# Kernel tuning notes

Measured on AMD Instinct MI355X. Metric: run time of the kernel, lower is better.

The kernel has to match this reference:

```python
import jax, jax.numpy as jnp
import numpy as np

INPUT_DIM = 784
LATENT_DIM = 32
HIDDEN = 256
NUM_PROTO = 25  # 5x5 SOM grid
BATCH = 65536


def setup_inputs() -> dict:
    key = jax.random.key(0)
    ks = jax.random.split(key, 10)
    s = lambda fan_in: 1.0 / np.sqrt(fan_in)
    return {
        "x": jax.random.uniform(ks[0], (BATCH, INPUT_DIM), dtype=jnp.float32),
        # encoder: Linear(784,256) -> ReLU -> Linear(256,32)
        "We1": jax.random.normal(ks[1], (INPUT_DIM, HIDDEN), dtype=jnp.float32) * s(INPUT_DIM),
        "be1": jnp.zeros((HIDDEN,), dtype=jnp.float32),
        "We2": jax.random.normal(ks[2], (HIDDEN, LATENT_DIM), dtype=jnp.float32) * s(HIDDEN),
        "be2": jnp.zeros((LATENT_DIM,), dtype=jnp.float32),
        # decoder: Linear(32,256) -> ReLU -> Linear(256,784) -> Sigmoid
        "Wd1": jax.random.normal(ks[3], (LATENT_DIM, HIDDEN), dtype=jnp.float32) * s(LATENT_DIM),
        "bd1": jnp.zeros((HIDDEN,), dtype=jnp.float32),
        "Wd2": jax.random.normal(ks[4], (HIDDEN, INPUT_DIM), dtype=jnp.float32) * s(HIDDEN),
        "bd2": jnp.zeros((INPUT_DIM,), dtype=jnp.float32),
        # SOM prototypes (torch.randn init)
        "prototypes": jax.random.normal(ks[5], (NUM_PROTO, LATENT_DIM), dtype=jnp.float32),
    }


def reference(x, We1, be1, We2, be2, Wd1, bd1, Wd2, bd2, prototypes):
    # encoder
    h = jax.nn.relu(x @ We1 + be1)          # [B, 256]
    z = h @ We2 + be2                        # [B, 32]
    # SOM layer: cdist -> argmin -> gather winning prototype
    # squared euclidean distance suffices for argmin
    sq_dists = (jnp.sum(z * z, axis=1, keepdims=True)
                - 2.0 * (z @ prototypes.T)
                + jnp.sum(prototypes * prototypes, axis=1))  # [B, 25]
    min_idx = jnp.argmin(sq_dists, axis=1)   # [B]
    som_z = prototypes[min_idx]              # [B, 32]
    # decoder
    hd = jax.nn.relu(som_z @ Wd1 + bd1)      # [B, 256]
    x_recon = jax.nn.sigmoid(hd @ Wd2 + bd2)  # [B, 784]
    return (x_recon, z, som_z)
```

## Files before the change

### kernel.cpp

```cpp
#include <hip/hip_runtime.h>
#include <hip/hip_bf16.h>
#include <math.h>

#define BATCH   65536
#define IN_DIM  784
#define HID     256
#define LAT     32
#define NPROTO  25

typedef short  short8  __attribute__((ext_vector_type(8)));
typedef float  floatx4 __attribute__((ext_vector_type(4)));

__device__ __forceinline__ unsigned short f2bf(float v) {
    __hip_bfloat16 b = __float2bfloat16(v);
    return *reinterpret_cast<unsigned short*>(&b);
}
__device__ __forceinline__ float bf2f(unsigned short u) {
    __hip_bfloat16 b = *reinterpret_cast<__hip_bfloat16*>(&u);
    return __bfloat162float(b);
}
__device__ __forceinline__ void split3(float v, unsigned short& o1,
                                       unsigned short& o2, unsigned short& o3) {
    o1 = f2bf(v); float r1 = v - bf2f(o1);
    o2 = f2bf(r1); float r2 = r1 - bf2f(o2);
    o3 = f2bf(r2);
}

__device__ __forceinline__ floatx4 mm_bf16(short8 a, short8 b, floatx4 c) {
    return __builtin_amdgcn_mfma_f32_16x16x32_bf16(a, b, c, 0, 0, 0);
}

__device__ __forceinline__ void async_copy16(const void* g, void* l) {
    __builtin_amdgcn_global_load_lds(
        (const __attribute__((address_space(1))) unsigned int*)g,
        (__attribute__((address_space(3))) unsigned int*)l, 16, 0, 0);
}

#define BT_BYTES   409600
#define WS_NEEDED  1307200

__global__ __launch_bounds__(256)
void prep_B(const float* __restrict__ We1,
            unsigned short* __restrict__ B1,
            unsigned short* __restrict__ B2,
            unsigned short* __restrict__ B3)
{
    int e = (blockIdx.x * 256 + threadIdx.x) * 4;
    int k = e & 31;
    int n = (e >> 5) & 255;
    int s = e >> 13;
    int cs = (k >> 3) ^ ((n >> 1) & 3);
    int dst = (s * 256 + n) * 32 + cs * 8 + (k & 7);
    ushort4 u1, u2, u3;
    unsigned short a, b, c;
#pragma unroll
    for (int j = 0; j < 4; ++j) {
        int kk = s * 32 + k + j;
        float v = (kk < IN_DIM) ? We1[(size_t)kk * HID + n] : 0.f;
        split3(v, a, b, c);
        ((unsigned short*)&u1)[j] = a;
        ((unsigned short*)&u2)[j] = b;
        ((unsigned short*)&u3)[j] = c;
    }
    *(ushort4*)(B1 + dst) = u1;
    *(ushort4*)(B2 + dst) = u2;
    *(ushort4*)(B3 + dst) = u3;
}

__global__ __launch_bounds__(256)
void dpsom_dectab(const float* __restrict__ protos,
                  const float* __restrict__ Wd1,
                  const float* __restrict__ bd1,
                  const float* __restrict__ Wd2,
                  const float* __restrict__ bd2,
                  float* __restrict__ table)
{
    __shared__ float pr[LAT];
    __shared__ float hd[HID];
    const int p = blockIdx.x;
    const int tid = threadIdx.x;
    if (tid < LAT) pr[tid] = protos[p * LAT + tid];
    __syncthreads();
    float s = bd1[tid];
#pragma unroll
    for (int k = 0; k < LAT; ++k)
        s = fmaf(pr[k], Wd1[k * HID + tid], s);
    hd[tid] = fmaxf(s, 0.f);
    __syncthreads();
    for (int i = tid; i < IN_DIM; i += 256) {
        float o = bd2[i];
        for (int j = 0; j < HID; ++j)
            o = fmaf(hd[j], Wd2[(size_t)j * IN_DIM + i], o);
        table[p * IN_DIM + i] = 1.f / (1.f + expf(-o));
    }
}

__global__ __launch_bounds__(256, 2)
void dpsom_encoder_mfma(const float* __restrict__ x,
                        const unsigned short* __restrict__ B1g,
                        const unsigned short* __restrict__ B2g,
                        const unsigned short* __restrict__ B3g,
                        const float* __restrict__ be1,
                        const float* __restrict__ We2,
                        const float* __restrict__ be2,
                        const float* __restrict__ protos,
                        const float* __restrict__ table,
                        float* __restrict__ z_out,
                        float* __restrict__ somz_out,
                        float* __restrict__ xrec)
{
    __shared__ __align__(16) char smem[61440];
    const int tid  = threadIdx.x;
    const int wave = tid >> 6;
    const int lane = tid & 63;
    const int l15  = lane & 15;
    const int q    = lane >> 4;
    const int sw   = (l15 >> 1) & 3;
    const int row0 = blockIdx.x * 64;

    floatx4 acc[4][4];
#pragma unroll
    for (int i = 0; i < 4; ++i)
#pragma unroll
        for (int j = 0; j < 4; ++j) acc[i][j] = (floatx4)0.f;

    for (int s = 0; s < 25; ++s) {
        __syncthreads();
        {
            size_t gbase = (size_t)s * 16384 + (size_t)wave * 4096 + (size_t)lane * 16;
            char* lb = smem + 12288 + wave * 4096 + lane * 16;
#pragma unroll
            for (int i = 0; i < 4; ++i) {
                async_copy16((const char*)B1g + gbase + i * 1024, lb + 0     + i * 1024);
                async_copy16((const char*)B2g + gbase + i * 1024, lb + 16384 + i * 1024);
                async_copy16((const char*)B3g + gbase + i * 1024, lb + 32768 + i * 1024);
            }
        }
#pragma unroll
        for (int i = 0; i < 2; ++i) {
            int ff  = tid + i * 256;
            int row = ff >> 3;
            int k4  = ff & 7;
            float4 v = make_float4(0.f, 0.f, 0.f, 0.f);
            if (s < 24 || k4 < 4)
                v = *(const float4*)(x + (size_t)(row0 + row) * IN_DIM + s * 32 + k4 * 4);
            ushort4 u1, u2, u3;
            unsigned short a, b, c;
            split3(v.x, a, b, c); u1.x = a; u2.x = b; u3.x = c;
            split3(v.y, a, b, c); u1.y = a; u2.y = b; u3.y = c;
            split3(v.z, a, b, c); u1.z = a; u2.z = b; u3.z = c;
            split3(v.w, a, b, c); u1.w = a; u2.w = b; u3.w = c;
            int csw = ((k4 >> 1) ^ ((row >> 1) & 3));
            int dst = row * 64 + csw * 16 + (k4 & 1) * 8;
            *(ushort4*)(smem + dst)        = u1;
            *(ushort4*)(smem + 4096 + dst) = u2;
            *(ushort4*)(smem + 8192 + dst) = u3;
        }
        __syncthreads();

        short8 afr[3][4];
#pragma unroll
        for (int mf = 0; mf < 4; ++mf) {
            int abyte = (16 * mf + l15) * 64 + ((q ^ sw) * 16);
            afr[0][mf] = *(short8*)(smem + abyte);
            afr[1][mf] = *(short8*)(smem + 4096 + abyte);
            afr[2][mf] = *(short8*)(smem + 8192 + abyte);
        }
#pragma unroll
        for (int nf = 0; nf < 4; ++nf) {
            int n = wave * 64 + 16 * nf + l15;
            int bbyte = n * 64 + ((q ^ sw) * 16);
            short8 b1 = *(short8*)(smem + 12288 + bbyte);
            short8 b2 = *(short8*)(smem + 28672 + bbyte);
            short8 b3 = *(short8*)(smem + 45056 + bbyte);
#pragma unroll
            for (int mf = 0; mf < 4; ++mf) {
                floatx4 t = acc[mf][nf];
                t = mm_bf16(afr[0][mf], b1, t);
                t = mm_bf16(afr[0][mf], b2, t);
                t = mm_bf16(afr[1][mf], b1, t);
                t = mm_bf16(afr[1][mf], b2, t);
                t = mm_bf16(afr[0][mf], b3, t);
                t = mm_bf16(afr[2][mf], b1, t);
                acc[mf][nf] = t;
            }
        }
    }

    {
        float bias[4];
#pragma unroll
        for (int nf = 0; nf < 4; ++nf) bias[nf] = be1[wave * 64 + 16 * nf + l15];
#pragma unroll
        for (int mf = 0; mf < 4; ++mf)
#pragma unroll
            for (int nf = 0; nf < 4; ++nf)
#pragma unroll
                for (int r = 0; r < 4; ++r)
                    acc[mf][nf][r] = fmaxf(acc[mf][nf][r] + bias[nf], 0.f);
    }

    float* h_lds = (float*)smem;
    float* z_lds = (float*)(smem + 33280);
    int*  minidx = (int*)(smem + 41728);

    const int jz = tid & 31;
    const int rg = tid >> 5;
    const float bz = be2[jz];

    for (int half = 0; half < 2; ++half) {
        __syncthreads();
#pragma unroll
        for (int mm = 0; mm < 2; ++mm) {
            int mf = 2 * half + mm;
#pragma unroll
            for (int nf = 0; nf < 4; ++nf)
#pragma unroll
                for (int r = 0; r < 4; ++r) {
                    int lr = 16 * mm + 4 * q + r;
                    h_lds[lr * 260 + wave * 64 + 16 * nf + l15] = acc[mf][nf][r];
                }
        }
        __syncthreads();
        float s0 = bz, s1 = bz, s2 = bz, s3 = bz;
        const float* h0p = h_lds + (rg * 4 + 0) * 260;
        const float* h1p = h_lds + (rg * 4 + 1) * 260;
        const float* h2p = h_lds + (rg * 4 + 2) * 260;
        const float* h3p = h_lds + (rg * 4 + 3) * 260;
#pragma unroll 4
        for (int c = 0; c < HID; c += 4) {
            float w0 = We2[(c + 0) * LAT + jz];
            float w1 = We2[(c + 1) * LAT + jz];
            float w2 = We2[(c + 2) * LAT + jz];
            float w3 = We2[(c + 3) * LAT + jz];
            float4 h0 = *(const float4*)(h0p + c);
            float4 h1 = *(const float4*)(h1p + c);
            float4 h2 = *(const float4*)(h2p + c);
            float4 h3 = *(const float4*)(h3p + c);
            s0 = fmaf(h0.x, w0, fmaf(h0.y, w1, fmaf(h0.z, w2, fmaf(h0.w, w3, s0))));
            s1 = fmaf(h1.x, w0, fmaf(h1.y, w1, fmaf(h1.z, w2, fmaf(h1.w, w3, s1))));
            s2 = fmaf(h2.x, w0, fmaf(h2.y, w1, fmaf(h2.z, w2, fmaf(h2.w, w3, s2))));
            s3 = fmaf(h3.x, w0, fmaf(h3.y, w1, fmaf(h3.z, w2, fmaf(h3.w, w3, s3))));
        }
        int rbase = half * 32 + rg * 4;
        z_lds[(rbase + 0) * 33 + jz] = s0;
        z_lds[(rbase + 1) * 33 + jz] = s1;
        z_lds[(rbase + 2) * 33 + jz] = s2;
        z_lds[(rbase + 3) * 33 + jz] = s3;
        z_out[(size_t)(row0 + rbase + 0) * LAT + jz] = s0;
        z_out[(size_t)(row0 + rbase + 1) * LAT + jz] = s1;
        z_out[(size_t)(row0 + rbase + 2) * LAT + jz] = s2;
        z_out[(size_t)(row0 + rbase + 3) * LAT + jz] = s3;
    }
    __syncthreads();

    if (tid < 64) {
        float zr[LAT];
        float zn = 0.f;
#pragma unroll
        for (int j = 0; j < LAT; ++j) {
            zr[j] = z_lds[tid * 33 + j];
            zn = fmaf(zr[j], zr[j], zn);
        }
        float best = 3.4e38f;
        int bp = 0;
        for (int p = 0; p < NPROTO; ++p) {
            float dot = 0.f, pn = 0.f;
#pragma unroll
            for (int j = 0; j < LAT; ++j) {
                float pv = protos[p * LAT + j];
                dot = fmaf(zr[j], pv, dot);
                pn  = fmaf(pv, pv, pn);
            }
            float d = zn - 2.f * dot + pn;
            if (d < best) { best = d; bp = p; }
        }
        minidx[tid] = bp;
    }
    __syncthreads();

#pragma unroll
    for (int m = 0; m < 8; ++m) {
        int r = rg * 8 + m;
        somz_out[(size_t)(row0 + r) * LAT + jz] = protos[minidx[r] * LAT + jz];
    }

    for (int i2 = tid; i2 < 64 * 196; i2 += 256) {
        int row = i2 / 196;
        int c   = i2 - row * 196;
        int idx = minidx[row];
        ((float4*)xrec)[(size_t)(row0 + row) * 196 + c] =
            ((const float4*)table)[idx * 196 + c];
    }
}

#define BMf 64
#define BKf 16
#define HSTRIDE 260
#define ZSTRIDE 33
#define SMEM_FLOATS 10432

__global__ __launch_bounds__(256)
void dpsom_encoder_fp32(const float* __restrict__ x,
                        const float* __restrict__ We1,
                        const float* __restrict__ be1,
                        const float* __restrict__ We2,
                        const float* __restrict__ be2,
                        const float* __restrict__ protos,
                        float* __restrict__ z_out,
                        float* __restrict__ somz_out,
                        int* __restrict__ minidx_out)
{
    __shared__ float smem[SMEM_FLOATS];
    __shared__ int minidx_lds[BMf];
    float* As = smem;
    float* Bs = smem + BKf * BMf;
    float* h_lds = smem;
    float* z_lds = smem + 32 * HSTRIDE;

    const int tid = threadIdx.x;
    const int tx = tid & 31;
    const int ty = tid >> 5;
    const int row0 = blockIdx.x * BMf;

    float acc[8][8];
#pragma unroll
    for (int i = 0; i < 8; ++i)
#pragma unroll
        for (int j = 0; j < 8; ++j) acc[i][j] = 0.f;

    const int ar  = tid >> 2;
    const int akq = tid & 3;

    for (int k0 = 0; k0 < IN_DIM; k0 += BKf) {
        __syncthreads();
        float4 av = *(const float4*)(x + (size_t)(row0 + ar) * IN_DIM + k0 + akq * 4);
        As[(akq * 4 + 0) * BMf + ar] = av.x;
        As[(akq * 4 + 1) * BMf + ar] = av.y;
        As[(akq * 4 + 2) * BMf + ar] = av.z;
        As[(akq * 4 + 3) * BMf + ar] = av.w;
#pragma unroll
        for (int i = 0; i < 4; ++i) {
            int f  = tid + i * 256;
            int bk = f >> 6;
            int bn = (f & 63) << 2;
            *(float4*)(Bs + bk * HID + bn) =
                *(const float4*)(We1 + (size_t)(k0 + bk) * HID + bn);
        }
        __syncthreads();
#pragma unroll
        for (int kk = 0; kk < BKf; ++kk) {
            float4 a0 = *(const float4*)(As + kk * BMf + ty * 8);
            float4 a1 = *(const float4*)(As + kk * BMf + ty * 8 + 4);
            float4 b0 = *(const float4*)(Bs + kk * HID + tx * 8);
            float4 b1 = *(const float4*)(Bs + kk * HID + tx * 8 + 4);
            float a[8] = {a0.x, a0.y, a0.z, a0.w, a1.x, a1.y, a1.z, a1.w};
            float b[8] = {b0.x, b0.y, b0.z, b0.w, b1.x, b1.y, b1.z, b1.w};
#pragma unroll
            for (int i = 0; i < 8; ++i)
#pragma unroll
                for (int j = 0; j < 8; ++j)
                    acc[i][j] = fmaf(a[i], b[j], acc[i][j]);
        }
    }
    {
        float bias[8];
#pragma unroll
        for (int j = 0; j < 8; ++j) bias[j] = be1[tx * 8 + j];
#pragma unroll
        for (int i = 0; i < 8; ++i)
#pragma unroll
            for (int j = 0; j < 8; ++j)
                acc[i][j] = fmaxf(acc[i][j] + bias[j], 0.f);
    }
    const int jz = tid & 31;
    const int rg = tid >> 5;
    const float bz = be2[jz];
    for (int half = 0; half < 2; ++half) {
        __syncthreads();
        if ((ty >> 2) == half) {
            int rb = (ty & 3) * 8;
#pragma unroll
            for (int i = 0; i < 8; ++i) {
                *(float4*)(h_lds + (rb + i) * HSTRIDE + tx * 8) =
                    make_float4(acc[i][0], acc[i][1], acc[i][2], acc[i][3]);
                *(float4*)(h_lds + (rb + i) * HSTRIDE + tx * 8 + 4) =
                    make_float4(acc[i][4], acc[i][5], acc[i][6], acc[i][7]);
            }
        }
        __syncthreads();
        float s0 = bz, s1 = bz, s2 = bz, s3 = bz;
        const float* h0p = h_lds + (rg * 4 + 0) * HSTRIDE;
        const float* h1p = h_lds + (rg * 4 + 1) * HSTRIDE;
        const float* h2p = h_lds + (rg * 4 + 2) * HSTRIDE;
        const float* h3p = h_lds + (rg * 4 + 3) * HSTRIDE;
#pragma unroll 4
        for (int c = 0; c < HID; c += 4) {
            float w0 = We2[(c + 0) * LAT + jz];
            float w1 = We2[(c + 1) * LAT + jz];
            float w2 = We2[(c + 2) * LAT + jz];
            float w3 = We2[(c + 3) * LAT + jz];
            float4 h0 = *(const float4*)(h0p + c);
            float4 h1 = *(const float4*)(h1p + c);
            float4 h2 = *(const float4*)(h2p + c);
            float4 h3 = *(const float4*)(h3p + c);
            s0 = fmaf(h0.x, w0, fmaf(h0.y, w1, fmaf(h0.z, w2, fmaf(h0.w, w3, s0))));
            s1 = fmaf(h1.x, w0, fmaf(h1.y, w1, fmaf(h1.z, w2, fmaf(h1.w, w3, s1))));
            s2 = fmaf(h2.x, w0, fmaf(h2.y, w1, fmaf(h2.z, w2, fmaf(h2.w, w3, s2))));
            s3 = fmaf(h3.x, w0, fmaf(h3.y, w1, fmaf(h3.z, w2, fmaf(h3.w, w3, s3))));
        }
        int rbase = half * 32 + rg * 4;
        z_lds[(rbase + 0) * ZSTRIDE + jz] = s0;
        z_lds[(rbase + 1) * ZSTRIDE + jz] = s1;
        z_lds[(rbase + 2) * ZSTRIDE + jz] = s2;
        z_lds[(rbase + 3) * ZSTRIDE + jz] = s3;
        z_out[(size_t)(row0 + rbase + 0) * LAT + jz] = s0;
        z_out[(size_t)(row0 + rbase + 1) * LAT + jz] = s1;
        z_out[(size_t)(row0 + rbase + 2) * LAT + jz] = s2;
        z_out[(size_t)(row0 + rbase + 3) * LAT + jz] = s3;
    }
    __syncthreads();
    if (tid < BMf) {
        float zr[LAT];
        float zn = 0.f;
#pragma unroll
        for (int j = 0; j < LAT; ++j) {
            zr[j] = z_lds[tid * ZSTRIDE + j];
            zn = fmaf(zr[j], zr[j], zn);
        }
        float best = 3.4e38f;
        int bp = 0;
        for (int p = 0; p < NPROTO; ++p) {
            float dot = 0.f, pn = 0.f;
#pragma unroll
            for (int j = 0; j < LAT; ++j) {
                float pv = protos[p * LAT + j];
                dot = fmaf(zr[j], pv, dot);
                pn  = fmaf(pv, pv, pn);
            }
            float d = zn - 2.f * dot + pn;
            if (d < best) { best = d; bp = p; }
        }
        minidx_out[row0 + tid] = bp;
        minidx_lds[tid] = bp;
    }
    __syncthreads();
#pragma unroll
    for (int m = 0; m < 8; ++m) {
        int r = rg * 8 + m;
        somz_out[(size_t)(row0 + r) * LAT + jz] = protos[minidx_lds[r] * LAT + jz];
    }
}

__global__ __launch_bounds__(256)
void dpsom_gather(const float4* __restrict__ table,
                  const int* __restrict__ minidx,
                  float4* __restrict__ xrec)
{
    const int f = blockIdx.x * 256 + threadIdx.x;
    const int row = f / 196;
    const int c4  = f - row * 196;
    const int idx = minidx[row];
    xrec[f] = table[idx * 196 + c4];
}

extern "C" void kernel_launch(void* const* d_in, const int* in_sizes, int n_in,
                              void* d_out, int out_size, void* d_ws, size_t ws_size,
                              hipStream_t stream)
{
    const float* x    = (const float*)d_in[0];
    const float* We1  = (const float*)d_in[1];
    const float* be1  = (const float*)d_in[2];
    const float* We2  = (const float*)d_in[3];
    const float* be2  = (const float*)d_in[4];
    const float* Wd1  = (const float*)d_in[5];
    const float* bd1  = (const float*)d_in[6];
    const float* Wd2  = (const float*)d_in[7];
    const float* bd2  = (const float*)d_in[8];
    const float* prot = (const float*)d_in[9];

    float* out   = (float*)d_out;
    float* xrec  = out;
    float* z_out = out + (size_t)BATCH * IN_DIM;
    float* somz  = z_out + (size_t)BATCH * LAT;

    if (ws_size >= WS_NEEDED) {
        unsigned short* B1 = (unsigned short*)d_ws;
        unsigned short* B2 = (unsigned short*)((char*)d_ws + BT_BYTES);
        unsigned short* B3 = (unsigned short*)((char*)d_ws + 2 * BT_BYTES);
        float* table = (float*)((char*)d_ws + 3 * BT_BYTES);

        hipLaunchKernelGGL(prep_B, dim3(200), dim3(256), 0, stream, We1, B1, B2, B3);
        hipLaunchKernelGGL(dpsom_dectab, dim3(NPROTO), dim3(256), 0, stream,
                           prot, Wd1, bd1, Wd2, bd2, table);
        hipLaunchKernelGGL(dpsom_encoder_mfma, dim3(BATCH / 64), dim3(256), 0, stream,
                           x, B1, B2, B3, be1, We2, be2, prot, table,
                           z_out, somz, xrec);
    } else {
        int*   minidx = (int*)d_ws;
        float* table  = (float*)((char*)d_ws + (size_t)BATCH * 4);
        hipLaunchKernelGGL(dpsom_encoder_fp32, dim3(BATCH / BMf), dim3(256), 0, stream,
                           x, We1, be1, We2, be2, prot, z_out, somz, minidx);
        hipLaunchKernelGGL(dpsom_dectab, dim3(NPROTO), dim3(256), 0, stream,
                           prot, Wd1, bd1, Wd2, bd2, table);
        hipLaunchKernelGGL(dpsom_gather, dim3((BATCH * (IN_DIM / 4)) / 256), dim3(256), 0, stream,
                           (const float4*)table, minidx, (float4*)xrec);
    }
}
```

Measured before the change: 516.0 us.

## Stream B fragments from global into registers and double-buffer A tiles in LDS

```diff
diff --git a/kernel.cpp b/kernel.cpp
--- a/kernel.cpp
+++ b/kernel.cpp
@@ -30,41 +30,37 @@
     return __builtin_amdgcn_mfma_f32_16x16x32_bf16(a, b, c, 0, 0, 0);
 }
 
-__device__ __forceinline__ void async_copy16(const void* g, void* l) {
-    __builtin_amdgcn_global_load_lds(
-        (const __attribute__((address_space(1))) unsigned int*)g,
-        (__attribute__((address_space(3))) unsigned int*)l, 16, 0, 0);
-}
-
-#define BT_BYTES   409600
+#define BT_SHORTS  204800
 #define WS_NEEDED  1307200
 
 __global__ __launch_bounds__(256)
-void prep_B(const float* __restrict__ We1,
-            unsigned short* __restrict__ B1,
-            unsigned short* __restrict__ B2,
-            unsigned short* __restrict__ B3)
+void prep_BF(const float* __restrict__ We1,
+             unsigned short* __restrict__ B1,
+             unsigned short* __restrict__ B2,
+             unsigned short* __restrict__ B3)
 {
-    int e = (blockIdx.x * 256 + threadIdx.x) * 4;
-    int k = e & 31;
-    int n = (e >> 5) & 255;
-    int s = e >> 13;
-    int cs = (k >> 3) ^ ((n >> 1) & 3);
-    int dst = (s * 256 + n) * 32 + cs * 8 + (k & 7);
-    ushort4 u1, u2, u3;
-    unsigned short a, b, c;
-#pragma unroll
-    for (int j = 0; j < 4; ++j) {
-        int kk = s * 32 + k + j;
-        float v = (kk < IN_DIM) ? We1[(size_t)kk * HID + n] : 0.f;
+    int t   = blockIdx.x * 256 + threadIdx.x;
+    int l15 = t & 15;
+    int q   = (t >> 4) & 3;
+    int sn  = t >> 6;
+    int s   = sn >> 4;
+    int n   = (sn & 15) * 16 + l15;
+    int k0  = s * 32 + q * 8;
+    short8 v1, v2, v3;
+#pragma unroll
+    for (int j = 0; j < 8; ++j) {
+        int k = k0 + j;
+        float v = (k < IN_DIM) ? We1[(size_t)k * HID + n] : 0.f;
+        unsigned short a, b, c;
         split3(v, a, b, c);
-        ((unsigned short*)&u1)[j] = a;
-        ((unsigned short*)&u2)[j] = b;
-        ((unsigned short*)&u3)[j] = c;
-    }
-    *(ushort4*)(B1 + dst) = u1;
-    *(ushort4*)(B2 + dst) = u2;
-    *(ushort4*)(B3 + dst) = u3;
+        v1[j] = (short)a;
+        v2[j] = (short)b;
+        v3[j] = (short)c;
+    }
+    size_t o = (size_t)t * 8;
+    *(short8*)(B1 + o) = v1;
+    *(short8*)(B2 + o) = v2;
+    *(short8*)(B3 + o) = v3;
 }
 
 __global__ __launch_bounds__(256)
@@ -95,96 +91,119 @@
     }
 }
 
-__global__ __launch_bounds__(256, 2)
-void dpsom_encoder_mfma(const float* __restrict__ x,
-                        const unsigned short* __restrict__ B1g,
-                        const unsigned short* __restrict__ B2g,
-                        const unsigned short* __restrict__ B3g,
-                        const float* __restrict__ be1,
-                        const float* __restrict__ We2,
-                        const float* __restrict__ be2,
-                        const float* __restrict__ protos,
-                        const float* __restrict__ table,
-                        float* __restrict__ z_out,
-                        float* __restrict__ somz_out,
-                        float* __restrict__ xrec)
+#define AST  80
+#define ABUF 15360
+
+__device__ __forceinline__ void cvt_write3(float4 v0, float4 v1, char* wp) {
+    float vv[8] = {v0.x, v0.y, v0.z, v0.w, v1.x, v1.y, v1.z, v1.w};
+    short8 u1, u2, u3;
+#pragma unroll
+    for (int j = 0; j < 8; ++j) {
+        unsigned short a, b, c;
+        split3(vv[j], a, b, c);
+        u1[j] = (short)a;
+        u2[j] = (short)b;
+        u3[j] = (short)c;
+    }
+    *(short8*)(wp)          = u1;
+    *(short8*)(wp + 5120)   = u2;
+    *(short8*)(wp + 10240)  = u3;
+}
+
+__global__ __launch_bounds__(256, 3)
+void dpsom_encoder_bf3(const float* __restrict__ x,
+                       const unsigned short* __restrict__ B1g,
+                       const unsigned short* __restrict__ B2g,
+                       const unsigned short* __restrict__ B3g,
+                       const float* __restrict__ be1,
+                       const float* __restrict__ We2,
+                       const float* __restrict__ be2,
+                       const float* __restrict__ protos,
+                       const float* __restrict__ table,
+                       float* __restrict__ z_out,
+                       float* __restrict__ somz_out,
+                       float* __restrict__ xrec)
 {
-    __shared__ __align__(16) char smem[61440];
+    __shared__ __align__(16) char smem[45056];
     const int tid  = threadIdx.x;
     const int wave = tid >> 6;
     const int lane = tid & 63;
     const int l15  = lane & 15;
     const int q    = lane >> 4;
-    const int sw   = (l15 >> 1) & 3;
     const int row0 = blockIdx.x * 64;
 
+    const int arow = tid >> 2;
+    const int aq   = tid & 3;
+    const float* xrow = x + (size_t)(row0 + arow) * IN_DIM + aq * 8;
+    char* awp = smem + arow * AST + aq * 16;
+
     floatx4 acc[4][4];
 #pragma unroll
     for (int i = 0; i < 4; ++i)
 #pragma unroll
         for (int j = 0; j < 4; ++j) acc[i][j] = (floatx4)0.f;
 
+    {
+        float4 v0 = *(const float4*)(xrow);
+        float4 v1 = *(const float4*)(xrow + 4);
+        cvt_write3(v0, v1, awp);
+    }
+    __syncthreads();
+
     for (int s = 0; s < 25; ++s) {
-        __syncthreads();
+        const char* abase = smem + (s & 1) * ABUF;
+        const int fb = (s * 16 + wave * 4) << 9;
+
+        short8 b1, b2, b3;
         {
-            size_t gbase = (size_t)s * 16384 + (size_t)wave * 4096 + (size_t)lane * 16;
-            char* lb = smem + 12288 + wave * 4096 + lane * 16;
-#pragma unroll
-            for (int i = 0; i < 4; ++i) {
-                async_copy16((const char*)B1g + gbase + i * 1024, lb + 0     + i * 1024);
-                async_copy16((const char*)B2g + gbase + i * 1024, lb + 16384 + i * 1024);
-                async_copy16((const char*)B3g + gbase + i * 1024, lb + 32768 + i * 1024);
+            int off0 = fb + (lane << 3);
+            b1 = *(const short8*)(B1g + off0);
+            b2 = *(const short8*)(B2g + off0);
+            b3 = *(const short8*)(B3g + off0);
+        }
+
+        float4 v0 = make_float4(0.f, 0.f, 0.f, 0.f), v1 = v0;
+        if (s < 24) {
+            if ((s < 23) | (aq < 2)) {
+                v0 = *(const float4*)(xrow + (s + 1) * 32);
+                v1 = *(const float4*)(xrow + (s + 1) * 32 + 4);
             }
         }
-#pragma unroll
-        for (int i = 0; i < 2; ++i) {
-            int ff  = tid + i * 256;
-            int row = ff >> 3;
-            int k4  = ff & 7;
-            float4 v = make_float4(0.f, 0.f, 0.f, 0.f);
-            if (s < 24 || k4 < 4)
-                v = *(const float4*)(x + (size_t)(row0 + row) * IN_DIM + s * 32 + k4 * 4);
-            ushort4 u1, u2, u3;
-            unsigned short a, b, c;
-            split3(v.x, a, b, c); u1.x = a; u2.x = b; u3.x = c;
-            split3(v.y, a, b, c); u1.y = a; u2.y = b; u3.y = c;
-            split3(v.z, a, b, c); u1.z = a; u2.z = b; u3.z = c;
-            split3(v.w, a, b, c); u1.w = a; u2.w = b; u3.w = c;
-            int csw = ((k4 >> 1) ^ ((row >> 1) & 3));
-            int dst = row * 64 + csw * 16 + (k4 & 1) * 8;
-            *(ushort4*)(smem + dst)        = u1;
-            *(ushort4*)(smem + 4096 + dst) = u2;
-            *(ushort4*)(smem + 8192 + dst) = u3;
-        }
-        __syncthreads();
-
-        short8 afr[3][4];
+
+        short8 a1f[4], a2f[4], a3f[4];
 #pragma unroll
         for (int mf = 0; mf < 4; ++mf) {
-            int abyte = (16 * mf + l15) * 64 + ((q ^ sw) * 16);
-            afr[0][mf] = *(short8*)(smem + abyte);
-            afr[1][mf] = *(short8*)(smem + 4096 + abyte);
-            afr[2][mf] = *(short8*)(smem + 8192 + abyte);
-        }
+            const char* ap = abase + (mf * 16 + l15) * AST + q * 16;
+            a1f[mf] = *(const short8*)ap;
+            a2f[mf] = *(const short8*)(ap + 5120);
+            a3f[mf] = *(const short8*)(ap + 10240);
+        }
+
+        if (s < 24) cvt_write3(v0, v1, awp + ((s + 1) & 1) * ABUF);
+
 #pragma unroll
         for (int nf = 0; nf < 4; ++nf) {
-            int n = wave * 64 + 16 * nf + l15;
-            int bbyte = n * 64 + ((q ^ sw) * 16);
-            short8 b1 = *(short8*)(smem + 12288 + bbyte);
-            short8 b2 = *(short8*)(smem + 28672 + bbyte);
-            short8 b3 = *(short8*)(smem + 45056 + bbyte);
-#pragma unroll
-            for (int mf = 0; mf < 4; ++mf) {
-                floatx4 t = acc[mf][nf];
-                t = mm_bf16(afr[0][mf], b1, t);
-                t = mm_bf16(afr[0][mf], b2, t);
-                t = mm_bf16(afr[1][mf], b1, t);
-                t = mm_bf16(afr[1][mf], b2, t);
-                t = mm_bf16(afr[0][mf], b3, t);
-                t = mm_bf16(afr[2][mf], b1, t);
-                acc[mf][nf] = t;
+            short8 cb1 = b1, cb2 = b2, cb3 = b3;
+            if (nf < 3) {
+                int offn = fb + ((nf + 1) << 9) + (lane << 3);
+                b1 = *(const short8*)(B1g + offn);
+                b2 = *(const short8*)(B2g + offn);
+                b3 = *(const short8*)(B3g + offn);
             }
-        }
+#pragma unroll
+            for (int mf = 0; mf < 4; ++mf) acc[mf][nf] = mm_bf16(a1f[mf], cb1, acc[mf][nf]);
+#pragma unroll
+            for (int mf = 0; mf < 4; ++mf) acc[mf][nf] = mm_bf16(a1f[mf], cb2, acc[mf][nf]);
+#pragma unroll
+            for (int mf = 0; mf < 4; ++mf) acc[mf][nf] = mm_bf16(a2f[mf], cb1, acc[mf][nf]);
+#pragma unroll
+            for (int mf = 0; mf < 4; ++mf) acc[mf][nf] = mm_bf16(a1f[mf], cb3, acc[mf][nf]);
+#pragma unroll
+            for (int mf = 0; mf < 4; ++mf) acc[mf][nf] = mm_bf16(a3f[mf], cb1, acc[mf][nf]);
+#pragma unroll
+            for (int mf = 0; mf < 4; ++mf) acc[mf][nf] = mm_bf16(a2f[mf], cb2, acc[mf][nf]);
+        }
+        __syncthreads();
     }
 
     {
@@ -200,19 +219,21 @@
                     acc[mf][nf][r] = fmaxf(acc[mf][nf][r] + bias[nf], 0.f);
     }
 
-    float* h_lds = (float*)smem;
-    float* z_lds = (float*)(smem + 33280);
-    int*  minidx = (int*)(smem + 41728);
+    float* h_lds  = (float*)smem;
+    float* z_lds  = (float*)(smem + 33280);
+    float* cdist  = (float*)(smem + 41728);
+    int*   cidx   = (int*)  (smem + 42752);
+    int*   minidx = (int*)  (smem + 43776);
 
     const int jz = tid & 31;
     const int rg = tid >> 5;
     const float bz = be2[jz];
 
-    for (int half = 0; half < 2; ++half) {
+    for (int hf = 0; hf < 2; ++hf) {
         __syncthreads();
 #pragma unroll
         for (int mm = 0; mm < 2; ++mm) {
-            int mf = 2 * half + mm;
+            int mf = 2 * hf + mm;
 #pragma unroll
             for (int nf = 0; nf < 4; ++nf)
 #pragma unroll
@@ -242,7 +263,7 @@
             s2 = fmaf(h2.x, w0, fmaf(h2.y, w1, fmaf(h2.z, w2, fmaf(h2.w, w3, s2))));
             s3 = fmaf(h3.x, w0, fmaf(h3.y, w1, fmaf(h3.z, w2, fmaf(h3.w, w3, s3))));
         }
-        int rbase = half * 32 + rg * 4;
+        int rbase = hf * 32 + rg * 4;
         z_lds[(rbase + 0) * 33 + jz] = s0;
         z_lds[(rbase + 1) * 33 + jz] = s1;
         z_lds[(rbase + 2) * 33 + jz] = s2;
@@ -254,17 +275,22 @@
     }
     __syncthreads();
 
-    if (tid < 64) {
+    {
+        const int r = tid & 63;
+        const int g = tid >> 6;
         float zr[LAT];
         float zn = 0.f;
 #pragma unroll
         for (int j = 0; j < LAT; ++j) {
-            zr[j] = z_lds[tid * 33 + j];
+            zr[j] = z_lds[r * 33 + j];
             zn = fmaf(zr[j], zr[j], zn);
         }
+        const int p0 = (g == 0) ? 0 : (1 + g * 6);
+        const int pc = (g == 0) ? 7 : 6;
         float best = 3.4e38f;
-        int bp = 0;
-        for (int p = 0; p < NPROTO; ++p) {
+        int bp = p0;
+        for (int pi = 0; pi < pc; ++pi) {
+            int p = p0 + pi;
             float dot = 0.f, pn = 0.f;
 #pragma unroll
             for (int j = 0; j < LAT; ++j) {
@@ -274,6 +300,18 @@
             }
             float d = zn - 2.f * dot + pn;
             if (d < best) { best = d; bp = p; }
+        }
+        cdist[r * 4 + g] = best;
+        cidx[r * 4 + g]  = bp;
+    }
+    __syncthreads();
+    if (tid < 64) {
+        float best = cdist[tid * 4];
+        int bp = cidx[tid * 4];
+#pragma unroll
+        for (int g = 1; g < 4; ++g) {
+            float d = cdist[tid * 4 + g];
+            if (d < best) { best = d; bp = cidx[tid * 4 + g]; }
         }
         minidx[tid] = bp;
     }
@@ -376,9 +414,9 @@
     const int jz = tid & 31;
     const int rg = tid >> 5;
     const float bz = be2[jz];
-    for (int half = 0; half < 2; ++half) {
-        __syncthreads();
-        if ((ty >> 2) == half) {
+    for (int hf = 0; hf < 2; ++hf) {
+        __syncthreads();
+        if ((ty >> 2) == hf) {
             int rb = (ty & 3) * 8;
 #pragma unroll
             for (int i = 0; i < 8; ++i) {
@@ -409,7 +447,7 @@
             s2 = fmaf(h2.x, w0, fmaf(h2.y, w1, fmaf(h2.z, w2, fmaf(h2.w, w3, s2))));
             s3 = fmaf(h3.x, w0, fmaf(h3.y, w1, fmaf(h3.z, w2, fmaf(h3.w, w3, s3))));
         }
-        int rbase = half * 32 + rg * 4;
+        int rbase = hf * 32 + rg * 4;
         z_lds[(rbase + 0) * ZSTRIDE + jz] = s0;
         z_lds[(rbase + 1) * ZSTRIDE + jz] = s1;
         z_lds[(rbase + 2) * ZSTRIDE + jz] = s2;
@@ -486,14 +524,14 @@
 
     if (ws_size >= WS_NEEDED) {
         unsigned short* B1 = (unsigned short*)d_ws;
-        unsigned short* B2 = (unsigned short*)((char*)d_ws + BT_BYTES);
-        unsigned short* B3 = (unsigned short*)((char*)d_ws + 2 * BT_BYTES);
-        float* table = (float*)((char*)d_ws + 3 * BT_BYTES);
-
-        hipLaunchKernelGGL(prep_B, dim3(200), dim3(256), 0, stream, We1, B1, B2, B3);
+        unsigned short* B2 = B1 + BT_SHORTS;
+        unsigned short* B3 = B2 + BT_SHORTS;
+        float* table = (float*)((char*)d_ws + 1228800);
+
+        hipLaunchKernelGGL(prep_BF, dim3(100), dim3(256), 0, stream, We1, B1, B2, B3);
         hipLaunchKernelGGL(dpsom_dectab, dim3(NPROTO), dim3(256), 0, stream,
                            prot, Wd1, bd1, Wd2, bd2, table);
-        hipLaunchKernelGGL(dpsom_encoder_mfma, dim3(BATCH / 64), dim3(256), 0, stream,
+        hipLaunchKernelGGL(dpsom_encoder_bf3, dim3(BATCH / 64), dim3(256), 0, stream,
                            x, B1, B2, B3, be1, We2, be2, prot, table,
                            z_out, somz, xrec);
     } else {
```

Result: slower. 527.3 us (+2.2%).
